# Optimization experiments

Measured on AMD Instinct MI355X. Metric: run time of the kernel, lower is better.

## Reference

```python
import jax, jax.numpy as jnp
import numpy as np

B, S, D, H, F, L = 16, 512, 512, 8, 2048, 3  # L layers: 1 in blocks_1 + 2 in blocks_2
DK = D // H
EPS = 1e-5

def setup_inputs():
    key = jax.random.key(0)
    ks = jax.random.split(key, 10)
    sc = 1.0 / np.sqrt(D)
    return dict(
        q_embed_data=jax.random.normal(ks[0], (B, S, D), jnp.float32),
        qa_embed_data=jax.random.normal(ks[1], (B, S, D), jnp.float32),
        Wk=jax.random.normal(ks[2], (L, D, D), jnp.float32) * sc,
        bk=jnp.zeros((L, D), jnp.float32),
        Wv=jax.random.normal(ks[3], (L, D, D), jnp.float32) * sc,
        bv=jnp.zeros((L, D), jnp.float32),
        Wo=jax.random.normal(ks[4], (L, D, D), jnp.float32) * sc,
        bo=jnp.zeros((L, D), jnp.float32),
        gammas=jax.random.normal(ks[5], (L, H, 1, 1), jnp.float32) * 0.5,
        ln1_g=jnp.ones((L, D), jnp.float32),
        ln1_b=jnp.zeros((L, D), jnp.float32),
        W1=jax.random.normal(ks[6], (L, D, F), jnp.float32) * sc,
        b1=jnp.zeros((L, F), jnp.float32),
        W2=jax.random.normal(ks[7], (L, F, D), jnp.float32) * (1.0 / np.sqrt(F)),
        b2=jnp.zeros((L, D), jnp.float32),
        ln2_g=jnp.ones((L, D), jnp.float32),
        ln2_b=jnp.zeros((L, D), jnp.float32),
    )

def _ln(x, g, b):
    m = jnp.mean(x, -1, keepdims=True)
    v = jnp.mean((x - m) ** 2, -1, keepdims=True)
    return (x - m) * jax.lax.rsqrt(v + EPS) * g + b

def _attention(q, k, v, mask, gamma):
    # q,k,v: [B,H,S,DK]; mask: [1,1,S,S] bool; gamma: [H,1,1]
    scores = jnp.einsum('bhid,bhjd->bhij', q, k) / np.sqrt(DK)
    maskf = mask.astype(scores.dtype)
    # first (no-grad in torch) softmax pass for distance decay
    p = jax.nn.softmax(jnp.where(mask, scores, -1e32), axis=-1) * maskf
    distcum = jnp.cumsum(p, axis=-1)
    disttot = jnp.sum(p, axis=-1, keepdims=True)
    idx = jnp.arange(scores.shape[-1])
    pos = jnp.abs(idx[None, :] - idx[:, None]).astype(scores.dtype)[None, None]
    dist = jax.lax.stop_gradient(
        jnp.sqrt(jnp.clip((disttot - distcum) * pos, 0.0, None)))
    g = -jax.nn.softplus(gamma)[None]  # [1,H,1,1]
    total_effect = jnp.clip(jnp.exp(dist * g), 1e-5, 1e5)
    scores = jnp.where(mask, scores * total_effect, -1e32)
    attn = jax.nn.softmax(scores, axis=-1)
    return jnp.einsum('bhij,bhjd->bhid', attn, v)

def _mha(q_in, k_in, v_in, mask, Wk, bk, Wv, bv, Wo, bo, gamma):
    bsz = q_in.shape[0]
    def proj(x, W, b):
        return (x @ W + b).reshape(bsz, -1, H, DK).transpose(0, 2, 1, 3)
    q = proj(q_in, Wk, bk)  # kq_same=True -> q uses k_linear
    k = proj(k_in, Wk, bk)
    v = proj(v_in, Wv, bv)
    o = _attention(q, k, v, mask, gamma)
    o = o.transpose(0, 2, 1, 3).reshape(bsz, -1, D)
    return o @ Wo + bo

def _block(i, mask, query, key, values, apply_pos, P):
    q2 = _mha(query, key, values, mask, P['Wk'][i], P['bk'][i], P['Wv'][i],
              P['bv'][i], P['Wo'][i], P['bo'][i], P['gammas'][i])
    x = _ln(query + q2, P['ln1_g'][i], P['ln1_b'][i])
    if apply_pos:
        h = jax.nn.relu(x @ P['W1'][i] + P['b1'][i]) @ P['W2'][i] + P['b2'][i]
        x = _ln(x + h, P['ln2_g'][i], P['ln2_b'][i])
    return x

def reference(q_embed_data, qa_embed_data, Wk, bk, Wv, bv, Wo, bo, gammas,
              ln1_g, ln1_b, W1, b1, W2, b2, ln2_g, ln2_b):
    P = dict(Wk=Wk, bk=bk, Wv=Wv, bv=bv, Wo=Wo, bo=bo, gammas=gammas,
             ln1_g=ln1_g, ln1_b=ln1_b, W1=W1, b1=b1, W2=W2, b2=b2,
             ln2_g=ln2_g, ln2_b=ln2_b)
    s = q_embed_data.shape[1]
    mask1 = jnp.tril(jnp.ones((s, s), bool))[None, None]        # mask==1: current+past
    mask0 = jnp.tril(jnp.ones((s, s), bool), -1)[None, None]    # mask==0: strictly past
    y = qa_embed_data
    x = q_embed_data
    y = _block(0, mask1, y, y, y, True, P)    # blocks_1: knowledge encoder
    x = _block(1, mask1, x, x, x, False, P)   # blocks_2: question encoder (no FFN)
    x = _block(2, mask0, x, x, y, True, P)    # blocks_2: knowledge retriever
    return x
```

## Files before the change

### kernel.cpp

```cpp
#include <hip/hip_runtime.h>
#include <hip/hip_bf16.h>

#define Bdim 16
#define Sdim 512
#define Ddim 512
#define Hdim 8
#define DKdim 64
#define Fdim 2048
#define Mrows (Bdim * Sdim)

typedef __attribute__((ext_vector_type(8))) short  frag16;
typedef __attribute__((ext_vector_type(4))) float  f32x4;
typedef __attribute__((ext_vector_type(8))) unsigned short ushort8;
typedef __attribute__((ext_vector_type(4))) unsigned short ushort4v;

#if defined(__has_builtin)
#  if __has_builtin(__builtin_amdgcn_exp2f)
#    define EXP2(x) __builtin_amdgcn_exp2f(x)
#  endif
#endif
#ifndef EXP2
#  define EXP2(x) __expf((x) * 0.6931471805599453f)
#endif
#define SC2 0.18033688011112042f

__device__ __forceinline__ unsigned short f2b(float x) {
    union { float f; unsigned int u; } v; v.f = x;
    unsigned int r = (v.u + 0x7FFFu + ((v.u >> 16) & 1u)) >> 16;
    return (unsigned short)r;
}

__global__ __launch_bounds__(256) void gemm_mfma(
    const __hip_bfloat16* __restrict__ A, const __hip_bfloat16* __restrict__ Bt,
    const float* __restrict__ bias, const float* __restrict__ R,
    float* __restrict__ Cf, unsigned short* __restrict__ Cb,
    int M, int N, int K, int do_relu)
{
    __shared__ short As[2][128 * 32];
    __shared__ short Bs[2][128 * 32];

    const int t = threadIdx.x;
    const int lane = t & 63;
    const int wave = t >> 6;

    const int gx = gridDim.x;
    const int nb = gx * gridDim.y;
    const int lid = blockIdx.x + gx * blockIdx.y;
    const int wid = (lid & 7) * (nb >> 3) + (lid >> 3);
    const int bm = (wid / gx) * 128;
    const int bn = (wid % gx) * 128;

    const int wm = (wave >> 1) * 64;
    const int wn = (wave & 1) * 64;

    f32x4 acc[4][4] = {};
    const int lrow = lane >> 2;
    const int lcol = (lane & 3) * 8;

    auto stage = [&](int k0, int buf) {
#pragma unroll
        for (int i = 0; i < 2; ++i) {
            const int chunk = wave * 2 + i;
            const int row = chunk * 16 + lrow;
            const __hip_bfloat16* ga = A + (size_t)(bm + row) * K + k0 + lcol;
            const __hip_bfloat16* gb = Bt + (size_t)(bn + row) * K + k0 + lcol;
            __builtin_amdgcn_global_load_lds(
                (const __attribute__((address_space(1))) unsigned int*)ga,
                (__attribute__((address_space(3))) unsigned int*)(&As[buf][chunk * 512]),
                16, 0, 0);
            __builtin_amdgcn_global_load_lds(
                (const __attribute__((address_space(1))) unsigned int*)gb,
                (__attribute__((address_space(3))) unsigned int*)(&Bs[buf][chunk * 512]),
                16, 0, 0);
        }
    };

    const int fr = lane & 15;
    const int quad = lane >> 4;
    const int nk = K >> 5;

    stage(0, 0);
    __syncthreads();

    for (int it = 0; it < nk; ++it) {
        const int buf = it & 1;
        if (it + 1 < nk) stage((it + 1) << 5, buf ^ 1);
        frag16 af[4], bfr[4];
#pragma unroll
        for (int i = 0; i < 4; ++i) {
            af[i]  = *(const frag16*)(&As[buf][(wm + i * 16 + fr) * 32 + quad * 8]);
            bfr[i] = *(const frag16*)(&Bs[buf][(wn + i * 16 + fr) * 32 + quad * 8]);
        }
#pragma unroll
        for (int mi = 0; mi < 4; ++mi)
#pragma unroll
            for (int ni = 0; ni < 4; ++ni)
                acc[mi][ni] = __builtin_amdgcn_mfma_f32_16x16x32_bf16(
                    af[mi], bfr[ni], acc[mi][ni], 0, 0, 0);
        __syncthreads();
    }

#pragma unroll
    for (int mi = 0; mi < 4; ++mi) {
#pragma unroll
        for (int r = 0; r < 4; ++r) {
            const int m = bm + wm + mi * 16 + quad * 4 + r;
#pragma unroll
            for (int ni = 0; ni < 4; ++ni) {
                const int n = bn + wn + ni * 16 + fr;
                float v = acc[mi][ni][r] + bias[n];
                if (R) v += R[(size_t)m * N + n];
                if (do_relu) v = fmaxf(v, 0.f);
                if (Cf) Cf[(size_t)m * N + n] = v;
                if (Cb) Cb[(size_t)m * N + n] = f2b(v);
            }
        }
    }
}

__global__ __launch_bounds__(256) void gemm_n64(
    const unsigned short* __restrict__ A0, const unsigned short* __restrict__ A1,
    const unsigned short* __restrict__ B0, const unsigned short* __restrict__ B1,
    const float* __restrict__ bias0, const float* __restrict__ bias1,
    const float* __restrict__ R, float* __restrict__ Cf,
    unsigned short* __restrict__ Cb, unsigned short* __restrict__ CbT,
    int K)
{
    const int NN = 512;
    __shared__ short As[2][128 * 32];
    __shared__ short Bs[2][64 * 32];

    const int trans = blockIdx.z;
    const unsigned short* A  = trans ? A1 : A0;
    const unsigned short* Bt = trans ? B1 : B0;
    const float* bias        = trans ? bias1 : bias0;

    const int t = threadIdx.x;
    const int lane = t & 63;
    const int wave = t >> 6;

    const int lid = blockIdx.x + 8 * blockIdx.y;
    const int wid = (lid & 7) * 64 + (lid >> 3);
    const int bm = (wid >> 3) * 128;
    const int bn = (wid & 7) * 64;

    const int wm = (wave >> 1) * 64;
    const int wn = (wave & 1) * 32;

    f32x4 acc[4][2] = {};
    const int lrow = lane >> 2;
    const int lcol = (lane & 3) * 8;

    auto stage = [&](int k0, int buf) {
#pragma unroll
        for (int i = 0; i < 2; ++i) {
            const int chunk = wave * 2 + i;
            const int row = chunk * 16 + lrow;
            const unsigned short* ga = A + (size_t)(bm + row) * K + k0 + lcol;
            __builtin_amdgcn_global_load_lds(
                (const __attribute__((address_space(1))) unsigned int*)ga,
                (__attribute__((address_space(3))) unsigned int*)(&As[buf][chunk * 512]),
                16, 0, 0);
        }
        {
            const int row = wave * 16 + lrow;
            const unsigned short* gb = Bt + (size_t)(bn + row) * K + k0 + lcol;
            __builtin_amdgcn_global_load_lds(
                (const __attribute__((address_space(1))) unsigned int*)gb,
                (__attribute__((address_space(3))) unsigned int*)(&Bs[buf][wave * 512]),
                16, 0, 0);
        }
    };

    const int fr = lane & 15;
    const int quad = lane >> 4;
    const int nk = K >> 5;

    stage(0, 0);
    __syncthreads();

    for (int it = 0; it < nk; ++it) {
        const int buf = it & 1;
        if (it + 1 < nk) stage((it + 1) << 5, buf ^ 1);
        frag16 af[4], bfr[2];
#pragma unroll
        for (int i = 0; i < 4; ++i)
            af[i] = *(const frag16*)(&As[buf][(wm + i * 16 + fr) * 32 + quad * 8]);
#pragma unroll
        for (int i = 0; i < 2; ++i)
            bfr[i] = *(const frag16*)(&Bs[buf][(wn + i * 16 + fr) * 32 + quad * 8]);
#pragma unroll
        for (int mi = 0; mi < 4; ++mi)
#pragma unroll
            for (int ni = 0; ni < 2; ++ni)
                acc[mi][ni] = __builtin_amdgcn_mfma_f32_16x16x32_bf16(
                    af[mi], bfr[ni], acc[mi][ni], 0, 0, 0);
        __syncthreads();
    }

    if (trans) {
#pragma unroll
        for (int mi = 0; mi < 4; ++mi)
#pragma unroll
            for (int ni = 0; ni < 2; ++ni) {
                const int m = bm + wm + mi * 16 + quad * 4;
                const int n = bn + wn + ni * 16 + fr;
                ushort4v o;
#pragma unroll
                for (int r = 0; r < 4; ++r) o[r] = f2b(acc[mi][ni][r] + bias[n]);
                const int bb = m >> 9, s = m & 511;
                const int hh = n >> 6, dd = n & 63;
                *(ushort4v*)(CbT + (((size_t)((bb * Hdim + hh) * DKdim + dd)) << 9) + s) = o;
            }
        return;
    }

#pragma unroll
    for (int mi = 0; mi < 4; ++mi) {
#pragma unroll
        for (int r = 0; r < 4; ++r) {
            const int m = bm + wm + mi * 16 + quad * 4 + r;
#pragma unroll
            for (int ni = 0; ni < 2; ++ni) {
                const int n = bn + wn + ni * 16 + fr;
                float v = acc[mi][ni][r] + bias[n];
                if (R) v += R[(size_t)m * NN + n];
                if (Cf) Cf[(size_t)m * NN + n] = v;
                if (Cb) Cb[(size_t)m * NN + n] = f2b(v);
            }
        }
    }
}

__global__ __launch_bounds__(256) void conv_b(
    const float* __restrict__ X, unsigned short* __restrict__ Y)
{
    const size_t i = ((size_t)blockIdx.x * 256 + threadIdx.x) * 8;
    float4 a = *(const float4*)(X + i);
    float4 b = *(const float4*)(X + i + 4);
    ushort8 o;
    o[0] = f2b(a.x); o[1] = f2b(a.y); o[2] = f2b(a.z); o[3] = f2b(a.w);
    o[4] = f2b(b.x); o[5] = f2b(b.y); o[6] = f2b(b.z); o[7] = f2b(b.w);
    *(ushort8*)(Y + i) = o;
}

__global__ __launch_bounds__(256) void wtrans_all(
    const float* __restrict__ Wk, const float* __restrict__ Wv,
    const float* __restrict__ Wo, const float* __restrict__ W1,
    const float* __restrict__ W2, unsigned short* __restrict__ dst)
{
    const int bid = blockIdx.x;
    const float* src; unsigned short* d; int K, N, tk, tn;
    if (bid < 576) {
        const int mat = bid >> 6, tile = bid & 63;
        const int l = mat / 3, wch = mat % 3;
        const float* W = (wch == 0) ? Wk : (wch == 1) ? Wv : Wo;
        src = W + (size_t)l * 262144;
        d = dst + (size_t)mat * 262144;
        K = 512; N = 512; tn = tile & 7; tk = tile >> 3;
    } else if (bid < 1088) {
        const int idx = bid - 576, l2 = idx >> 8, tile = idx & 255;
        src = W1 + (size_t)(l2 * 2) * (512 * 2048);
        d = dst + 9 * 262144 + (size_t)l2 * (512 * 2048);
        K = 512; N = 2048; tn = tile & 31; tk = tile >> 5;
    } else {
        const int idx = bid - 1088, l2 = idx >> 8, tile = idx & 255;
        src = W2 + (size_t)(l2 * 2) * (2048 * 512);
        d = dst + 9 * 262144 + 2 * (512 * 2048) + (size_t)l2 * (2048 * 512);
        K = 2048; N = 512; tn = tile & 7; tk = tile >> 3;
    }
    const int n0 = tn * 64, k0 = tk * 64;
    __shared__ float T[64][65];
    const int t = threadIdx.x;
    const int kl = t >> 4, n4 = (t & 15) << 2;
#pragma unroll
    for (int it = 0; it < 4; ++it) {
        const int k = kl + it * 16;
        float4 v = *(const float4*)(src + (size_t)(k0 + k) * N + n0 + n4);
        T[n4 + 0][k] = v.x; T[n4 + 1][k] = v.y;
        T[n4 + 2][k] = v.z; T[n4 + 3][k] = v.w;
    }
    __syncthreads();
    const int nl = t >> 3, k8 = (t & 7) << 3;
#pragma unroll
    for (int it = 0; it < 2; ++it) {
        const int n = nl + it * 32;
        ushort8 o;
#pragma unroll
        for (int c = 0; c < 8; ++c) o[c] = f2b(T[n][k8 + c]);
        *(ushort8*)(d + (size_t)(n0 + n) * K + k0 + k8) = o;
    }
}

__global__ __launch_bounds__(128, 4) void attn_flash7(
    const unsigned short* __restrict__ Kb,
    const unsigned short* __restrict__ Vt,
    const float* __restrict__ gam,
    unsigned short* __restrict__ Ob,
    int mask_type)
{
    __shared__ float CTw[16 * 33];
    __shared__ unsigned short Pst[2][16 * 36];
    __shared__ float S1s[2][16];
    __shared__ float S2s[2][16];
    __shared__ float OaccS[16 * 66];

    const int h = blockIdx.y, b = blockIdx.z;
    const int t = threadIdx.x, lane = t & 63, p = t >> 6;
    const int quad = lane >> 4, fr = lane & 15;

    const unsigned short* kbase = Kb + (size_t)b * Sdim * Ddim + h * DKdim;
    const unsigned short* vtb = Vt + (size_t)(b * Hdim + h) * DKdim * Sdim;
    const float gneg2 = -log1pf(__expf(gam[h])) * 1.4426950408889634f;

    for (int half_t = 0; half_t < 2; ++half_t) {
        const int tile = half_t ? (31 - blockIdx.x) : blockIdx.x;
        const int q0 = tile * 16;
        const int iRow = q0 + fr;

        frag16 aq0 = *(const frag16*)(kbase + (size_t)(q0 + fr) * Ddim + quad * 8);
        frag16 aq1 = *(const frag16*)(kbase + (size_t)(q0 + fr) * Ddim + 32 + quad * 8);

        float psum = 0.f;
        for (int jn = p; jn <= tile; jn += 2) {
            frag16 k0 = *(const frag16*)(kbase + (size_t)(jn * 16 + fr) * Ddim + quad * 8);
            frag16 k1 = *(const frag16*)(kbase + (size_t)(jn * 16 + fr) * Ddim + 32 + quad * 8);
            f32x4 z = {0.f, 0.f, 0.f, 0.f};
            z = __builtin_amdgcn_mfma_f32_16x16x32_bf16(k0, aq0, z, 0, 0, 0);
            z = __builtin_amdgcn_mfma_f32_16x16x32_bf16(k1, aq1, z, 0, 0, 0);
            float tq = 0.f;
            if (jn < tile) {
#pragma unroll
                for (int r = 0; r < 4; ++r) tq += EXP2(z[r] * SC2);
            } else {
#pragma unroll
                for (int r = 0; r < 4; ++r) {
                    const bool valid = mask_type ? (quad * 4 + r <= fr)
                                                 : (quad * 4 + r < fr);
                    tq += valid ? EXP2(z[r] * SC2) : 0.f;
                }
            }
            psum += tq;
            float tt = tq;
            tt += __shfl_xor(tt, 16);
            tt += __shfl_xor(tt, 32);
            if (quad == 0) CTw[fr * 33 + jn] = tt;
        }
        {
            float s1 = psum;
            s1 += __shfl_xor(s1, 16);
            s1 += __shfl_xor(s1, 32);
            if (lane < 16) S1s[p][lane] = s1;
        }
        __syncthreads();

        if (p == 0 && lane < 16) {
            float run = 0.f;
            for (int jn = tile; jn >= 0; --jn) {
                const float tv = CTw[lane * 33 + jn];
                CTw[lane * 33 + jn] = run;
                run += tv;
            }
        }
        __syncthreads();

        const float rsum1 = 1.f / (S1s[0][fr] + S1s[1][fr]);
        unsigned short* Pw = Pst[p];
        const bool fm_blk = (mask_type == 0) && (tile == 0);
        const bool fmrow = fm_blk && (fr == 0);
        const int umax = fm_blk ? (Sdim / 32 - 1) : (tile >> 1);
        float sum2p = 0.f;
        f32x4 oacc[4] = {};

        for (int u = umax - p; u >= 0; u -= 2) {
#pragma unroll
            for (int half = 0; half < 2; ++half) {
                const int jn = 2 * u + half;
                uint2 pku;
                if (jn > tile) {
                    const unsigned int pv = fmrow ? 0x3F803F80u : 0u;
                    pku.x = pv; pku.y = pv;
                    sum2p += fmrow ? 4.f : 0.f;
                } else {
                    frag16 k0 = *(const frag16*)(kbase + (size_t)(jn * 16 + fr) * Ddim + quad * 8);
                    frag16 k1 = *(const frag16*)(kbase + (size_t)(jn * 16 + fr) * Ddim + 32 + quad * 8);
                    f32x4 z = {0.f, 0.f, 0.f, 0.f};
                    z = __builtin_amdgcn_mfma_f32_16x16x32_bf16(k0, aq0, z, 0, 0, 0);
                    z = __builtin_amdgcn_mfma_f32_16x16x32_bf16(k1, aq1, z, 0, 0, 0);
                    const bool full = (jn < tile);
                    float s2r[4], lsuf[4];
                    float tq = 0.f;
#pragma unroll
                    for (int r = 3; r >= 0; --r) {
                        lsuf[r] = tq;
                        s2r[r] = z[r] * SC2;
                        float e1 = EXP2(s2r[r]);
                        if (!full) {
                            const bool valid = mask_type ? (quad * 4 + r <= fr)
                                                         : (quad * 4 + r < fr);
                            e1 = valid ? e1 : 0.f;
                        }
                        tq += e1;
                    }
                    float incl = tq;
                    {
                        float u1 = __shfl_down(incl, 16);
                        incl += (quad < 3) ? u1 : 0.f;
                        float u2 = __shfl_down(incl, 32);
                        incl += (quad < 2) ? u2 : 0.f;
                    }
                    const float base = CTw[fr * 33 + jn] + (incl - tq);
                    const float pos0 = (float)(iRow - (jn * 16 + quad * 4));
                    float e2v[4];
#pragma unroll
                    for (int r = 0; r < 4; ++r) {
                        const float ratio = (base + lsuf[r]) * rsum1;
                        const float arg = ratio * fabsf(pos0 - (float)r);
                        const float te = fmaxf(EXP2(gneg2 * sqrtf(arg)), 1e-5f);
                        float e2 = EXP2(s2r[r] * te);
                        if (!full) {
                            const bool valid = mask_type ? (quad * 4 + r <= fr)
                                                         : (quad * 4 + r < fr);
                            e2 = valid ? e2 : (fmrow ? 1.f : 0.f);
                        }
                        sum2p += e2;
                        e2v[r] = e2;
                    }
                    union { __hip_bfloat162 hh; unsigned int u; } c0, c1;
                    c0.hh = __float22bfloat162_rn(make_float2(e2v[0], e2v[1]));
                    c1.hh = __float22bfloat162_rn(make_float2(e2v[2], e2v[3]));
                    pku.x = c0.u; pku.y = c1.u;
                }
                *(uint2*)(Pw + fr * 36 + half * 16 + quad * 4) = pku;
            }
            frag16 pf = *(const frag16*)(Pw + fr * 36 + quad * 8);
            const int jb = u * 32;
#pragma unroll
            for (int dt = 0; dt < 4; ++dt) {
                frag16 vf = *(const frag16*)(vtb + (size_t)(dt * 16 + fr) * Sdim + jb + quad * 8);
                oacc[dt] = __builtin_amdgcn_mfma_f32_16x16x32_bf16(pf, vf, oacc[dt], 0, 0, 0);
            }
        }

        {
            float s2 = sum2p;
            s2 += __shfl_xor(s2, 16);
            s2 += __shfl_xor(s2, 32);
            if (lane < 16) S2s[p][lane] = s2;
        }
        if (p == 1) {
#pragma unroll
            for (int dt = 0; dt < 4; ++dt)
#pragma unroll
                for (int r = 0; r < 4; ++r)
                    OaccS[(quad * 4 + r) * 66 + dt * 16 + fr] = oacc[dt][r];
        }
        __syncthreads();

        if (p == 0) {
            const float rs2 = 1.f / (S2s[0][fr] + S2s[1][fr]);
            float rs2q[4];
#pragma unroll
            for (int r = 0; r < 4; ++r) rs2q[r] = __shfl(rs2, quad * 4 + r);

            unsigned short* obase = Ob + ((size_t)(b * Sdim + q0)) * Ddim + h * DKdim;
#pragma unroll
            for (int dt = 0; dt < 4; ++dt)
#pragma unroll
                for (int r = 0; r < 4; ++r) {
                    const float v = oacc[dt][r] + OaccS[(quad * 4 + r) * 66 + dt * 16 + fr];
                    obase[(size_t)(quad * 4 + r) * Ddim + dt * 16 + fr] = f2b(v * rs2q[r]);
                }
        }
    }
}

__global__ __launch_bounds__(256) void ln_kernel(
    const float* __restrict__ X, const float* __restrict__ g,
    const float* __restrict__ bta, float* __restrict__ Y,
    unsigned short* __restrict__ Yb)
{
    const int row = blockIdx.x;
    const int t = threadIdx.x;
    __shared__ float r1[256], r2[256];
    const float* x = X + (size_t)row * Ddim;
    float a = x[t], b = x[t + 256];
    r1[t] = a + b;
    r2[t] = a * a + b * b;
    __syncthreads();
    for (int off = 128; off; off >>= 1) {
        if (t < off) { r1[t] += r1[t + off]; r2[t] += r2[t + off]; }
        __syncthreads();
    }
    float mean = r1[0] * (1.f / Ddim);
    float var = r2[0] * (1.f / Ddim) - mean * mean;
    float rs = rsqrtf(var + 1e-5f);
    float y0 = (a - mean) * rs * g[t] + bta[t];
    float y1 = (b - mean) * rs * g[t + 256] + bta[t + 256];
    if (Y) {
        float* y = Y + (size_t)row * Ddim;
        y[t] = y0;
        y[t + 256] = y1;
    }
    if (Yb) {
        unsigned short* yb = Yb + (size_t)row * Ddim;
        yb[t] = f2b(y0);
        yb[t + 256] = f2b(y1);
    }
}

extern "C" void kernel_launch(void* const* d_in, const int* in_sizes, int n_in,
                              void* d_out, int out_size, void* d_ws, size_t ws_size,
                              hipStream_t stream)
{
    const float* x0     = (const float*)d_in[0];
    const float* y0     = (const float*)d_in[1];
    const float* Wk     = (const float*)d_in[2];
    const float* bk     = (const float*)d_in[3];
    const float* Wv     = (const float*)d_in[4];
    const float* bv     = (const float*)d_in[5];
    const float* Wo     = (const float*)d_in[6];
    const float* bo     = (const float*)d_in[7];
    const float* gammas = (const float*)d_in[8];
    const float* ln1g   = (const float*)d_in[9];
    const float* ln1b   = (const float*)d_in[10];
    const float* W1     = (const float*)d_in[11];
    const float* b1     = (const float*)d_in[12];
    const float* W2     = (const float*)d_in[13];
    const float* b2     = (const float*)d_in[14];
    const float* ln2g   = (const float*)d_in[15];
    const float* ln2b   = (const float*)d_in[16];

    const size_t NBSD = (size_t)Mrows * Ddim;
    float* ws = (float*)d_ws;
    float* T1   = ws;
    float* X1   = T1 + NBSD;
    float* Xbuf = X1 + NBSD;
    unsigned short* Kbf = (unsigned short*)(Xbuf + NBSD);
    unsigned short* Vt  = Kbf + NBSD;
    unsigned short* AOb = Vt + NBSD;
    unsigned short* Abf = AOb + NBSD;
    unsigned short* Xbf = Abf + NBSD;
    unsigned short* Ybf = Xbf + NBSD;
    unsigned short* Hbb = Ybf + NBSD;
    unsigned short* WtAll = Hbb + (size_t)Mrows * Fdim;

    auto WtK = [&](int l) { return WtAll + (size_t)(l * 3 + 0) * 262144; };
    auto WtV = [&](int l) { return WtAll + (size_t)(l * 3 + 1) * 262144; };
    auto WtO = [&](int l) { return WtAll + (size_t)(l * 3 + 2) * 262144; };
    auto Wt1 = [&](int l) { return WtAll + 9 * 262144 + (size_t)(l >> 1) * (512 * 2048); };
    auto Wt2 = [&](int l) { return WtAll + 9 * 262144 + 2 * (512 * 2048) + (size_t)(l >> 1) * (2048 * 512); };

    const int convBlocks = (int)(NBSD / 2048);

    wtrans_all<<<1600, 256, 0, stream>>>(Wk, Wv, Wo, W1, W2, WtAll);

    auto run_block = [&](int l, const float* qinf, const unsigned short* qinb,
                         const unsigned short* vinb, int mask_type, bool ffn,
                         float* outf, unsigned short* outb) {
        const float* bk_l = bk + (size_t)l * Ddim;
        const float* bv_l = bv + (size_t)l * Ddim;
        const float* bo_l = bo + (size_t)l * Ddim;

        gemm_n64<<<dim3(8, 64, 2), 256, 0, stream>>>(
            qinb, vinb, WtK(l), WtV(l), bk_l, bv_l,
            nullptr, nullptr, Kbf, Vt, Ddim);
        attn_flash7<<<dim3(16, Hdim, Bdim), 128, 0, stream>>>(
            Kbf, Vt, gammas + (size_t)l * Hdim, AOb, mask_type);
        gemm_n64<<<dim3(8, 64, 1), 256, 0, stream>>>(
            AOb, AOb, WtO(l), WtO(l), bo_l, bo_l,
            qinf, T1, nullptr, nullptr, Ddim);
        float* x1f = ffn ? X1 : outf;
        unsigned short* x1b = ffn ? Abf : outb;
        ln_kernel<<<Mrows, 256, 0, stream>>>(T1,
            ln1g + (size_t)l * Ddim, ln1b + (size_t)l * Ddim, x1f, x1b);
        if (ffn) {
            const float* b1_l = b1 + (size_t)l * Fdim;
            const float* b2_l = b2 + (size_t)l * Ddim;
            gemm_mfma<<<dim3(Fdim / 128, Mrows / 128), 256, 0, stream>>>(
                (const __hip_bfloat16*)Abf, (const __hip_bfloat16*)Wt1(l),
                b1_l, nullptr, nullptr, Hbb, Mrows, Fdim, Ddim, 1);
            gemm_n64<<<dim3(8, 64, 1), 256, 0, stream>>>(
                Hbb, Hbb, Wt2(l), Wt2(l), b2_l, b2_l,
                X1, T1, nullptr, nullptr, Fdim);
            ln_kernel<<<Mrows, 256, 0, stream>>>(T1,
                ln2g + (size_t)l * Ddim, ln2b + (size_t)l * Ddim, outf, outb);
        }
    };

    conv_b<<<convBlocks, 256, 0, stream>>>(y0, Abf);
    run_block(0, y0, Abf, Abf, 1, true, nullptr, Ybf);
    conv_b<<<convBlocks, 256, 0, stream>>>(x0, Abf);
    run_block(1, x0, Abf, Abf, 1, false, Xbuf, Xbf);
    run_block(2, Xbuf, Xbf, Ybf, 0, true, (float*)d_out, nullptr);
}
```

Before: 646.4 us.

## Split attention into one 4-wave block per query tile, heaviest tiles first

The attention kernel changes from 2-wave blocks that each process a pair of mirrored query tiles to 4-wave blocks that each handle a single query tile. The grid order puts the longest causal tiles first, and partial output accumulators from the four waves are reduced through shared memory. The goal is more parallelism, more waves per key range and better load balance across CUs. The cost is an extra reduction stage with more barriers, twice the shared-memory P staging, and heavier per-block setup, since the Q fragment load is no longer shared by two tiles.

```diff
diff --git a/kernel.cpp b/kernel.cpp
--- a/kernel.cpp
+++ b/kernel.cpp
@@ -292,7 +292,7 @@
     }
 }
 
-__global__ __launch_bounds__(128, 4) void attn_flash7(
+__global__ __launch_bounds__(256, 8) void attn_flash8(
     const unsigned short* __restrict__ Kb,
     const unsigned short* __restrict__ Vt,
     const float* __restrict__ gam,
@@ -300,178 +300,208 @@
     int mask_type)
 {
     __shared__ float CTw[16 * 33];
-    __shared__ unsigned short Pst[2][16 * 36];
-    __shared__ float S1s[2][16];
-    __shared__ float S2s[2][16];
-    __shared__ float OaccS[16 * 66];
-
-    const int h = blockIdx.y, b = blockIdx.z;
-    const int t = threadIdx.x, lane = t & 63, p = t >> 6;
+    __shared__ unsigned short Pst[4][16 * 36];
+    __shared__ float S1s[4][16];
+    __shared__ float S2s[4][16];
+    __shared__ float OaccA[16 * 66];
+    __shared__ float OaccB[16 * 66];
+
+    const int h = blockIdx.x & 7, b = blockIdx.x >> 3;
+    const int rk = blockIdx.y;
+    const int tile = mask_type ? (31 - rk) : (rk == 0 ? 0 : 32 - rk);
+
+    const int t = threadIdx.x, lane = t & 63, w = t >> 6;
     const int quad = lane >> 4, fr = lane & 15;
+    const int q0 = tile * 16;
+    const int iRow = q0 + fr;
 
     const unsigned short* kbase = Kb + (size_t)b * Sdim * Ddim + h * DKdim;
     const unsigned short* vtb = Vt + (size_t)(b * Hdim + h) * DKdim * Sdim;
     const float gneg2 = -log1pf(__expf(gam[h])) * 1.4426950408889634f;
 
-    for (int half_t = 0; half_t < 2; ++half_t) {
-        const int tile = half_t ? (31 - blockIdx.x) : blockIdx.x;
-        const int q0 = tile * 16;
-        const int iRow = q0 + fr;
-
-        frag16 aq0 = *(const frag16*)(kbase + (size_t)(q0 + fr) * Ddim + quad * 8);
-        frag16 aq1 = *(const frag16*)(kbase + (size_t)(q0 + fr) * Ddim + 32 + quad * 8);
-
-        float psum = 0.f;
-        for (int jn = p; jn <= tile; jn += 2) {
-            frag16 k0 = *(const frag16*)(kbase + (size_t)(jn * 16 + fr) * Ddim + quad * 8);
-            frag16 k1 = *(const frag16*)(kbase + (size_t)(jn * 16 + fr) * Ddim + 32 + quad * 8);
-            f32x4 z = {0.f, 0.f, 0.f, 0.f};
-            z = __builtin_amdgcn_mfma_f32_16x16x32_bf16(k0, aq0, z, 0, 0, 0);
-            z = __builtin_amdgcn_mfma_f32_16x16x32_bf16(k1, aq1, z, 0, 0, 0);
-            float tq = 0.f;
-            if (jn < tile) {
-#pragma unroll
-                for (int r = 0; r < 4; ++r) tq += EXP2(z[r] * SC2);
+    frag16 aq0 = *(const frag16*)(kbase + (size_t)(q0 + fr) * Ddim + quad * 8);
+    frag16 aq1 = *(const frag16*)(kbase + (size_t)(q0 + fr) * Ddim + 32 + quad * 8);
+
+    float psum = 0.f;
+    for (int jn = w; jn <= tile; jn += 4) {
+        frag16 k0 = *(const frag16*)(kbase + (size_t)(jn * 16 + fr) * Ddim + quad * 8);
+        frag16 k1 = *(const frag16*)(kbase + (size_t)(jn * 16 + fr) * Ddim + 32 + quad * 8);
+        f32x4 z = {0.f, 0.f, 0.f, 0.f};
+        z = __builtin_amdgcn_mfma_f32_16x16x32_bf16(k0, aq0, z, 0, 0, 0);
+        z = __builtin_amdgcn_mfma_f32_16x16x32_bf16(k1, aq1, z, 0, 0, 0);
+        float tq = 0.f;
+        if (jn < tile) {
+#pragma unroll
+            for (int r = 0; r < 4; ++r) tq += EXP2(z[r] * SC2);
+        } else {
+#pragma unroll
+            for (int r = 0; r < 4; ++r) {
+                const bool valid = mask_type ? (quad * 4 + r <= fr)
+                                             : (quad * 4 + r < fr);
+                tq += valid ? EXP2(z[r] * SC2) : 0.f;
+            }
+        }
+        psum += tq;
+        float tt = tq;
+        tt += __shfl_xor(tt, 16);
+        tt += __shfl_xor(tt, 32);
+        if (quad == 0) CTw[fr * 33 + jn] = tt;
+    }
+    {
+        float s1 = psum;
+        s1 += __shfl_xor(s1, 16);
+        s1 += __shfl_xor(s1, 32);
+        if (lane < 16) S1s[w][lane] = s1;
+    }
+    __syncthreads();
+
+    if (w == 0 && lane < 16) {
+        float run = 0.f;
+        for (int jn = tile; jn >= 0; --jn) {
+            const float tv = CTw[lane * 33 + jn];
+            CTw[lane * 33 + jn] = run;
+            run += tv;
+        }
+    }
+    __syncthreads();
+
+    const float rsum1 = 1.f / (S1s[0][fr] + S1s[1][fr] + S1s[2][fr] + S1s[3][fr]);
+    unsigned short* Pw = Pst[w];
+    const bool fm_blk = (mask_type == 0) && (tile == 0);
+    const bool fmrow = fm_blk && (fr == 0);
+    const int umax = fm_blk ? (Sdim / 32 - 1) : (tile >> 1);
+    float sum2p = 0.f;
+    f32x4 oacc[4] = {};
+
+    for (int u = umax - w; u >= 0; u -= 4) {
+#pragma unroll
+        for (int half = 0; half < 2; ++half) {
+            const int jn = 2 * u + half;
+            uint2 pku;
+            if (jn > tile) {
+                const unsigned int pv = fmrow ? 0x3F803F80u : 0u;
+                pku.x = pv; pku.y = pv;
+                sum2p += fmrow ? 4.f : 0.f;
             } else {
+                frag16 k0 = *(const frag16*)(kbase + (size_t)(jn * 16 + fr) * Ddim + quad * 8);
+                frag16 k1 = *(const frag16*)(kbase + (size_t)(jn * 16 + fr) * Ddim + 32 + quad * 8);
+                f32x4 z = {0.f, 0.f, 0.f, 0.f};
+                z = __builtin_amdgcn_mfma_f32_16x16x32_bf16(k0, aq0, z, 0, 0, 0);
+                z = __builtin_amdgcn_mfma_f32_16x16x32_bf16(k1, aq1, z, 0, 0, 0);
+                const bool full = (jn < tile);
+                float s2r[4], lsuf[4];
+                float tq = 0.f;
+#pragma unroll
+                for (int r = 3; r >= 0; --r) {
+                    lsuf[r] = tq;
+                    s2r[r] = z[r] * SC2;
+                    float e1 = EXP2(s2r[r]);
+                    if (!full) {
+                        const bool valid = mask_type ? (quad * 4 + r <= fr)
+                                                     : (quad * 4 + r < fr);
+                        e1 = valid ? e1 : 0.f;
+                    }
+                    tq += e1;
+                }
+                float incl = tq;
+                {
+                    float u1 = __shfl_down(incl, 16);
+                    incl += (quad < 3) ? u1 : 0.f;
+                    float u2 = __shfl_down(incl, 32);
+                    incl += (quad < 2) ? u2 : 0.f;
+                }
+                const float base = CTw[fr * 33 + jn] + (incl - tq);
+                const float pos0 = (float)(iRow - (jn * 16 + quad * 4));
+                float e2v[4];
 #pragma unroll
                 for (int r = 0; r < 4; ++r) {
-                    const bool valid = mask_type ? (quad * 4 + r <= fr)
-                                                 : (quad * 4 + r < fr);
-                    tq += valid ? EXP2(z[r] * SC2) : 0.f;
+                    const float ratio = (base + lsuf[r]) * rsum1;
+                    const float arg = ratio * fabsf(pos0 - (float)r);
+                    const float te = fmaxf(EXP2(gneg2 * sqrtf(arg)), 1e-5f);
+                    float e2 = EXP2(s2r[r] * te);
+                    if (!full) {
+                        const bool valid = mask_type ? (quad * 4 + r <= fr)
+                                                     : (quad * 4 + r < fr);
+                        e2 = valid ? e2 : (fmrow ? 1.f : 0.f);
+                    }
+                    sum2p += e2;
+                    e2v[r] = e2;
                 }
+                union { __hip_bfloat162 hh; unsigned int u; } c0, c1;
+                c0.hh = __float22bfloat162_rn(make_float2(e2v[0], e2v[1]));
+                c1.hh = __float22bfloat162_rn(make_float2(e2v[2], e2v[3]));
+                pku.x = c0.u; pku.y = c1.u;
             }
-            psum += tq;
-            float tt = tq;
-            tt += __shfl_xor(tt, 16);
-            tt += __shfl_xor(tt, 32);
-            if (quad == 0) CTw[fr * 33 + jn] = tt;
-        }
-        {
-            float s1 = psum;
-            s1 += __shfl_xor(s1, 16);
-            s1 += __shfl_xor(s1, 32);
-            if (lane < 16) S1s[p][lane] = s1;
-        }
-        __syncthreads();
-
-        if (p == 0 && lane < 16) {
-            float run = 0.f;
-            for (int jn = tile; jn >= 0; --jn) {
-                const float tv = CTw[lane * 33 + jn];
-                CTw[lane * 33 + jn] = run;
-                run += tv;
+            *(uint2*)(Pw + fr * 36 + half * 16 + quad * 4) = pku;
+        }
+        frag16 pf = *(const frag16*)(Pw + fr * 36 + quad * 8);
+        const int jb = u * 32;
+#pragma unroll
+        for (int dt = 0; dt < 4; ++dt) {
+            frag16 vf = *(const frag16*)(vtb + (size_t)(dt * 16 + fr) * Sdim + jb + quad * 8);
+            oacc[dt] = __builtin_amdgcn_mfma_f32_16x16x32_bf16(pf, vf, oacc[dt], 0, 0, 0);
+        }
+    }
+
+    {
+        float s2 = sum2p;
+        s2 += __shfl_xor(s2, 16);
+        s2 += __shfl_xor(s2, 32);
+        if (lane < 16) S2s[w][lane] = s2;
+    }
+    if (w == 1) {
+#pragma unroll
+        for (int dt = 0; dt < 4; ++dt)
+#pragma unroll
+            for (int r = 0; r < 4; ++r)
+                OaccA[(quad * 4 + r) * 66 + dt * 16 + fr] = oacc[dt][r];
+    }
+    if (w == 3) {
+#pragma unroll
+        for (int dt = 0; dt < 4; ++dt)
+#pragma unroll
+            for (int r = 0; r < 4; ++r)
+                OaccB[(quad * 4 + r) * 66 + dt * 16 + fr] = oacc[dt][r];
+    }
+    __syncthreads();
+    if (w == 0) {
+#pragma unroll
+        for (int dt = 0; dt < 4; ++dt)
+#pragma unroll
+            for (int r = 0; r < 4; ++r)
+                oacc[dt][r] += OaccA[(quad * 4 + r) * 66 + dt * 16 + fr];
+    }
+    if (w == 2) {
+#pragma unroll
+        for (int dt = 0; dt < 4; ++dt)
+#pragma unroll
+            for (int r = 0; r < 4; ++r)
+                oacc[dt][r] += OaccB[(quad * 4 + r) * 66 + dt * 16 + fr];
+    }
+    __syncthreads();
+    if (w == 2) {
+#pragma unroll
+        for (int dt = 0; dt < 4; ++dt)
+#pragma unroll
+            for (int r = 0; r < 4; ++r)
+                OaccA[(quad * 4 + r) * 66 + dt * 16 + fr] = oacc[dt][r];
+    }
+    __syncthreads();
+
+    if (w == 0) {
+        const float rs2 = 1.f / (S2s[0][fr] + S2s[1][fr] + S2s[2][fr] + S2s[3][fr]);
+        float rs2q[4];
+#pragma unroll
+        for (int r = 0; r < 4; ++r) rs2q[r] = __shfl(rs2, quad * 4 + r);
+
+        unsigned short* obase = Ob + ((size_t)(b * Sdim + q0)) * Ddim + h * DKdim;
+#pragma unroll
+        for (int dt = 0; dt < 4; ++dt)
+#pragma unroll
+            for (int r = 0; r < 4; ++r) {
+                const float v = oacc[dt][r] + OaccA[(quad * 4 + r) * 66 + dt * 16 + fr];
+                obase[(size_t)(quad * 4 + r) * Ddim + dt * 16 + fr] = f2b(v * rs2q[r]);
             }
-        }
-        __syncthreads();
-
-        const float rsum1 = 1.f / (S1s[0][fr] + S1s[1][fr]);
-        unsigned short* Pw = Pst[p];
-        const bool fm_blk = (mask_type == 0) && (tile == 0);
-        const bool fmrow = fm_blk && (fr == 0);
-        const int umax = fm_blk ? (Sdim / 32 - 1) : (tile >> 1);
-        float sum2p = 0.f;
-        f32x4 oacc[4] = {};
-
-        for (int u = umax - p; u >= 0; u -= 2) {
-#pragma unroll
-            for (int half = 0; half < 2; ++half) {
-                const int jn = 2 * u + half;
-                uint2 pku;
-                if (jn > tile) {
-                    const unsigned int pv = fmrow ? 0x3F803F80u : 0u;
-                    pku.x = pv; pku.y = pv;
-                    sum2p += fmrow ? 4.f : 0.f;
-                } else {
-                    frag16 k0 = *(const frag16*)(kbase + (size_t)(jn * 16 + fr) * Ddim + quad * 8);
-                    frag16 k1 = *(const frag16*)(kbase + (size_t)(jn * 16 + fr) * Ddim + 32 + quad * 8);
-                    f32x4 z = {0.f, 0.f, 0.f, 0.f};
-                    z = __builtin_amdgcn_mfma_f32_16x16x32_bf16(k0, aq0, z, 0, 0, 0);
-                    z = __builtin_amdgcn_mfma_f32_16x16x32_bf16(k1, aq1, z, 0, 0, 0);
-                    const bool full = (jn < tile);
-                    float s2r[4], lsuf[4];
-                    float tq = 0.f;
-#pragma unroll
-                    for (int r = 3; r >= 0; --r) {
-                        lsuf[r] = tq;
-                        s2r[r] = z[r] * SC2;
-                        float e1 = EXP2(s2r[r]);
-                        if (!full) {
-                            const bool valid = mask_type ? (quad * 4 + r <= fr)
-                                                         : (quad * 4 + r < fr);
-                            e1 = valid ? e1 : 0.f;
-                        }
-                        tq += e1;
-                    }
-                    float incl = tq;
-                    {
-                        float u1 = __shfl_down(incl, 16);
-                        incl += (quad < 3) ? u1 : 0.f;
-                        float u2 = __shfl_down(incl, 32);
-                        incl += (quad < 2) ? u2 : 0.f;
-                    }
-                    const float base = CTw[fr * 33 + jn] + (incl - tq);
-                    const float pos0 = (float)(iRow - (jn * 16 + quad * 4));
-                    float e2v[4];
-#pragma unroll
-                    for (int r = 0; r < 4; ++r) {
-                        const float ratio = (base + lsuf[r]) * rsum1;
-                        const float arg = ratio * fabsf(pos0 - (float)r);
-                        const float te = fmaxf(EXP2(gneg2 * sqrtf(arg)), 1e-5f);
-                        float e2 = EXP2(s2r[r] * te);
-                        if (!full) {
-                            const bool valid = mask_type ? (quad * 4 + r <= fr)
-                                                         : (quad * 4 + r < fr);
-                            e2 = valid ? e2 : (fmrow ? 1.f : 0.f);
-                        }
-                        sum2p += e2;
-                        e2v[r] = e2;
-                    }
-                    union { __hip_bfloat162 hh; unsigned int u; } c0, c1;
-                    c0.hh = __float22bfloat162_rn(make_float2(e2v[0], e2v[1]));
-                    c1.hh = __float22bfloat162_rn(make_float2(e2v[2], e2v[3]));
-                    pku.x = c0.u; pku.y = c1.u;
-                }
-                *(uint2*)(Pw + fr * 36 + half * 16 + quad * 4) = pku;
-            }
-            frag16 pf = *(const frag16*)(Pw + fr * 36 + quad * 8);
-            const int jb = u * 32;
-#pragma unroll
-            for (int dt = 0; dt < 4; ++dt) {
-                frag16 vf = *(const frag16*)(vtb + (size_t)(dt * 16 + fr) * Sdim + jb + quad * 8);
-                oacc[dt] = __builtin_amdgcn_mfma_f32_16x16x32_bf16(pf, vf, oacc[dt], 0, 0, 0);
-            }
-        }
-
-        {
-            float s2 = sum2p;
-            s2 += __shfl_xor(s2, 16);
-            s2 += __shfl_xor(s2, 32);
-            if (lane < 16) S2s[p][lane] = s2;
-        }
-        if (p == 1) {
-#pragma unroll
-            for (int dt = 0; dt < 4; ++dt)
-#pragma unroll
-                for (int r = 0; r < 4; ++r)
-                    OaccS[(quad * 4 + r) * 66 + dt * 16 + fr] = oacc[dt][r];
-        }
-        __syncthreads();
-
-        if (p == 0) {
-            const float rs2 = 1.f / (S2s[0][fr] + S2s[1][fr]);
-            float rs2q[4];
-#pragma unroll
-            for (int r = 0; r < 4; ++r) rs2q[r] = __shfl(rs2, quad * 4 + r);
-
-            unsigned short* obase = Ob + ((size_t)(b * Sdim + q0)) * Ddim + h * DKdim;
-#pragma unroll
-            for (int dt = 0; dt < 4; ++dt)
-#pragma unroll
-                for (int r = 0; r < 4; ++r) {
-                    const float v = oacc[dt][r] + OaccS[(quad * 4 + r) * 66 + dt * 16 + fr];
-                    obase[(size_t)(quad * 4 + r) * Ddim + dt * 16 + fr] = f2b(v * rs2q[r]);
-                }
-        }
     }
 }
 
@@ -565,7 +595,7 @@
         gemm_n64<<<dim3(8, 64, 2), 256, 0, stream>>>(
             qinb, vinb, WtK(l), WtV(l), bk_l, bv_l,
             nullptr, nullptr, Kbf, Vt, Ddim);
-        attn_flash7<<<dim3(16, Hdim, Bdim), 128, 0, stream>>>(
+        attn_flash8<<<dim3(Bdim * Hdim, Sdim / 16, 1), 256, 0, stream>>>(
             Kbf, Vt, gammas + (size_t)l * Hdim, AOb, mask_type);
         gemm_n64<<<dim3(8, 64, 1), 256, 0, stream>>>(
             AOb, AOb, WtO(l), WtO(l), bo_l, bo_l,
```

After: 627.7 us. -2.9%, faster.
